# Optimization experiments

Hardware: AMD Instinct MI355X
Metric: run time of the kernel (lower is better)

The kernel has to match this reference:

```python
import jax, jax.numpy as jnp
import numpy as np

M = 28            # mask head resolution (mask_logit[i] is MxM)
NUM_CLASSES = 80  # max value of cls_idx (mask_image channel count)


def setup_inputs() -> dict:
    key = jax.random.key(0)
    k1, k2, k3, k4, k5, k6, k7 = jax.random.split(key, 7)
    N, H, W = 100, 800, 800
    cx = jax.random.uniform(k1, (N,), minval=0.0, maxval=float(W - 1))
    cy = jax.random.uniform(k2, (N,), minval=0.0, maxval=float(H - 1))
    bw = jax.random.uniform(k3, (N,), minval=20.0, maxval=300.0)
    bh = jax.random.uniform(k4, (N,), minval=20.0, maxval=300.0)
    mask_rois = jnp.stack([cx - bw / 2, cy - bh / 2, cx + bw / 2, cy + bh / 2], axis=1).astype(jnp.float32)
    cls_prob = jax.random.uniform(k5, (N,), dtype=jnp.float32)
    mask_prob = jax.random.normal(k6, (N, M, M), dtype=jnp.float32)
    cls_idx = jax.random.randint(k7, (N,), 1, NUM_CLASSES + 1, dtype=jnp.int32)
    return {"mask_rois": mask_rois, "cls_prob": cls_prob, "mask_prob": mask_prob,
            "cls_idx": cls_idx, "im_h": H, "im_w": W}


def _paste(logit, box, H, W):
    """Bilinear-paste an MxM logit into the full HxW image (== cv2.resize to (w,h)
    then placing at the box, evaluated directly on image pixel coords)."""
    x0, y0, x1, y1 = box[0], box[1], box[2], box[3]  # int32
    w = jnp.maximum(x1 - x0 + 1, 1).astype(jnp.float32)
    h = jnp.maximum(y1 - y0 + 1, 1).astype(jnp.float32)
    xs = jnp.arange(W, dtype=jnp.float32)
    ys = jnp.arange(H, dtype=jnp.float32)
    # cv2 bilinear mapping: src = (dst + 0.5) * (M / size) - 0.5, clamped at borders
    sx = jnp.clip((xs - x0.astype(jnp.float32) + 0.5) * (M / w) - 0.5, 0.0, M - 1.0)
    sy = jnp.clip((ys - y0.astype(jnp.float32) + 0.5) * (M / h) - 0.5, 0.0, M - 1.0)
    ix0 = jnp.floor(sx).astype(jnp.int32); ix1 = jnp.minimum(ix0 + 1, M - 1); fx = sx - ix0
    iy0 = jnp.floor(sy).astype(jnp.int32); iy1 = jnp.minimum(iy0 + 1, M - 1); fy = sy - iy0
    v00 = logit[iy0[:, None], ix0[None, :]]
    v01 = logit[iy0[:, None], ix1[None, :]]
    v10 = logit[iy1[:, None], ix0[None, :]]
    v11 = logit[iy1[:, None], ix1[None, :]]
    val = ((1 - fy)[:, None] * ((1 - fx)[None, :] * v00 + fx[None, :] * v01)
           + fy[:, None] * ((1 - fx)[None, :] * v10 + fx[None, :] * v11))
    xi = jnp.arange(W, dtype=jnp.int32)
    yi = jnp.arange(H, dtype=jnp.int32)
    inside_x = (xi >= jnp.maximum(x0, 0)) & (xi < jnp.minimum(x1 + 1, W))
    inside_y = (yi >= jnp.maximum(y0, 0)) & (yi < jnp.minimum(y1 + 1, H))
    inside = inside_y[:, None] & inside_x[None, :]
    return jnp.where(inside, val, 0.0), inside


def _forward(mask_rois, cls_prob, mask_prob, cls_idx, H, W, thr):
    N = mask_prob.shape[0]
    order = jnp.argsort(-cls_prob)                       # sort by score, descending
    boxes = mask_rois[order].astype(jnp.int32)
    logits = mask_prob[order]
    cls = cls_idx[order].astype(jnp.int32) - 1           # 0-based class ids
    pasted, inside = jax.vmap(lambda l, b: _paste(l, b, H, W))(logits, boxes)  # [N,H,W]

    def step(mask_image, xs):
        logit, ins, c = xs
        mask = (logit > 0) & ins                          # thresholded, in-image crop mask
        prev = mask_image[c]
        msum = jnp.sum(mask).astype(jnp.float32)
        ovl = jnp.sum(mask & prev).astype(jnp.float32)    # overlap with accumulated class mask
        keep = (msum > 0) & (ovl <= thr * msum)           # skip if ratio > threshold
        mask_image = mask_image.at[c].set(prev | (mask & keep))
        return mask_image, keep

    mask_image0 = jnp.zeros((NUM_CLASSES, H, W), dtype=bool)
    _, keep = jax.lax.scan(step, mask_image0, (pasted, inside, cls))

    # compact kept masks to the front (frame_id order); dropped boxes go to slot N (discarded)
    pos = jnp.where(keep, jnp.cumsum(keep.astype(jnp.int32)) - 1, N)
    energy = jnp.where(inside & keep[:, None, None], pasted, 0.0)
    full = jnp.zeros((N + 1, H, W), pasted.dtype).at[pos].set(energy)
    mask_energy = full[:N][None]                          # [1, N, H, W], kept masks first
    keep_inds = jnp.full((N + 1,), -1, jnp.int32).at[pos].set(
        jnp.where(keep, order.astype(jnp.int32), -1))[:N]
    return keep_inds, mask_energy


def reference(mask_rois, cls_prob, mask_prob, cls_idx, im_h, im_w):
    return _forward(mask_rois, cls_prob, mask_prob, cls_idx, int(im_h), int(im_w), 0.3)
```

## Files before the change

kernel.cpp:

```cpp
#include <hip/hip_runtime.h>

#define NINST 100
#define MLOG 28
#define IMG 800
#define LOGSZ (MLOG * MLOG)

#define OFF_ORDER 0
#define OFF_CLS   100
#define OFF_BOX   200
#define OFF_MSUM  600
#define OFF_SLOT  800
#define OFF_NK    900
#define OFF_MASK  1024
#define ROWW      12
#define MSTRIDE   (ROWW * 304)
#define PAIR_CAP  512
#define ZTOT      (IMG * IMG * NINST / 4)
#define ZBLKS     4096

__global__ __launch_bounds__(256) void k_raster(const float* __restrict__ mask_prob,
                                                const float* __restrict__ cls_prob,
                                                const float* __restrict__ rois,
                                                const int* __restrict__ cls_idx,
                                                int* __restrict__ ws) {
    int b = blockIdx.x, tid = threadIdx.x;
    __shared__ float s_p[NINST];
    __shared__ int s_order[NINST];
    __shared__ float lg[LOGSZ];
    __shared__ int red[256];
    if (tid < NINST) s_p[tid] = cls_prob[tid];
    __syncthreads();
    if (tid < NINST) {
        float p = s_p[tid];
        int r = 0;
        for (int j = 0; j < NINST; j++) {
            float q = s_p[j];
            r += (q > p) || (q == p && j < tid);
        }
        s_order[r] = tid;
    }
    __syncthreads();
    int n = b;
    int orig = s_order[n];
    int x0 = (int)rois[4 * orig], y0 = (int)rois[4 * orig + 1];
    int x1 = (int)rois[4 * orig + 2], y1 = (int)rois[4 * orig + 3];
    if (b == 0) {
        if (tid < NINST) {
            int o = s_order[tid];
            ws[OFF_ORDER + tid] = o;
            ws[OFF_CLS + tid] = cls_idx[o] - 1;
#pragma unroll
            for (int k = 0; k < 4; k++)
                ws[OFF_BOX + 4 * tid + k] = (int)rois[4 * o + k];
        }
    }
    for (int i = tid; i < LOGSZ; i += 256) lg[i] = mask_prob[orig * LOGSZ + i];
    __syncthreads();
    int xs = max(x0, 0), xe = min(x1 + 1, IMG);
    int ys = max(y0, 0), ye = min(y1 + 1, IMG);
    int wx0 = xs >> 5, nw = ((xe + 31) >> 5) - wx0, nrows = ye - ys;
    float wf = fmaxf((float)(x1 - x0 + 1), 1.f), hf = fmaxf((float)(y1 - y0 + 1), 1.f);
    float rx = 28.f / wf, ry = 28.f / hf;
    unsigned* mb = (unsigned*)(ws + OFF_MASK) + n * MSTRIDE;
    int total = nrows * nw, cnt = 0;
    for (int t = tid; t < total; t += 256) {
        int row = t / nw, wc = t - row * nw;
        int y = ys + row;
        float sy = ((float)y - (float)y0 + 0.5f) * ry - 0.5f;
        sy = fminf(fmaxf(sy, 0.f), 27.f);
        int iy0 = (int)sy, iy1 = min(iy0 + 1, 27);
        float fy = sy - (float)iy0;
        const float* r0 = lg + iy0 * MLOG;
        const float* r1 = lg + iy1 * MLOG;
        unsigned bits = 0u;
        int xbase = (wx0 + wc) << 5;
        int j0 = max(xs - xbase, 0), j1 = min(xe - xbase, 32);
        for (int j = j0; j < j1; j++) {
            int xx = xbase + j;
            float sx = ((float)xx - (float)x0 + 0.5f) * rx - 0.5f;
            sx = fminf(fmaxf(sx, 0.f), 27.f);
            int ix0 = (int)sx, ix1 = min(ix0 + 1, 27);
            float fx = sx - (float)ix0;
            float val = (1.f - fy) * ((1.f - fx) * r0[ix0] + fx * r0[ix1]) +
                        fy * ((1.f - fx) * r1[ix0] + fx * r1[ix1]);
            bits |= (val > 0.f) ? (1u << j) : 0u;
        }
        mb[row * ROWW + wc] = bits;
        cnt += __popc(bits);
    }
    red[tid] = cnt;
    __syncthreads();
    for (int s = 128; s; s >>= 1) {
        if (tid < s) red[tid] += red[tid + s];
        __syncthreads();
    }
    if (tid == 0) ws[OFF_MSUM + n] = red[0];
}

__global__ __launch_bounds__(256) void k_scan_zero(int* __restrict__ ws, float* __restrict__ out) {
    int b = blockIdx.x, tid = threadIdx.x;
    if (b > 0) {
        float4* z = (float4*)(out + NINST);
        for (size_t pi = (size_t)(b - 1) * 256 + tid; pi < (size_t)ZTOT; pi += (size_t)ZBLKS * 256)
            z[pi] = make_float4(0.f, 0.f, 0.f, 0.f);
        return;
    }
    const unsigned* maskbase = (const unsigned*)(ws + OFF_MASK);
    __shared__ int s_cls[NINST], s_msum[NINST], s_box[4 * NINST];
    __shared__ int s_wi[PAIR_CAP], s_wj[PAIR_CAP], s_po[PAIR_CAP];
    __shared__ int s_nw;
    __shared__ int s_cand[32];
    for (int i = tid; i < NINST; i += 256) {
        s_cls[i] = ws[OFF_CLS + i];
        s_msum[i] = ws[OFF_MSUM + i];
    }
    for (int i = tid; i < 4 * NINST; i += 256) s_box[i] = ws[OFF_BOX + i];
    if (tid == 0) s_nw = 0;
    __syncthreads();
    for (int c = tid; c < NINST * NINST; c += 256) {
        int i = c / NINST, j = c - i * NINST;
        if (i >= j) continue;
        if (s_cls[i] != s_cls[j]) continue;
        if (s_msum[i] == 0 || s_msum[j] == 0) continue;
        int ixs = max(s_box[4 * i], 0), ixe = min(s_box[4 * i + 2] + 1, IMG);
        int iys = max(s_box[4 * i + 1], 0), iye = min(s_box[4 * i + 3] + 1, IMG);
        int jxs = max(s_box[4 * j], 0), jxe = min(s_box[4 * j + 2] + 1, IMG);
        int jys = max(s_box[4 * j + 1], 0), jye = min(s_box[4 * j + 3] + 1, IMG);
        if (!(ixs < jxe && jxs < ixe && iys < jye && jys < iye)) continue;
        int k = atomicAdd(&s_nw, 1);
        if (k < PAIR_CAP) { s_wi[k] = i; s_wj[k] = j; }
    }
    __syncthreads();
    int nw = min(s_nw, PAIR_CAP);
    int wid = tid >> 6, lane = tid & 63;
    for (int k = wid; k < nw; k += 4) {
        int i = s_wi[k], j = s_wj[k];
        int ixs = max(s_box[4 * i], 0), ixe = min(s_box[4 * i + 2] + 1, IMG);
        int iys = max(s_box[4 * i + 1], 0), iye = min(s_box[4 * i + 3] + 1, IMG);
        int jxs = max(s_box[4 * j], 0), jxe = min(s_box[4 * j + 2] + 1, IMG);
        int jys = max(s_box[4 * j + 1], 0);
        int iwx0 = ixs >> 5, jwx0 = jxs >> 5;
        int wlo = max(iwx0, jwx0);
        int whi = min((ixe + 31) >> 5, (jxe + 31) >> 5);
        int rlo = max(iys, jys);
        int rhi = min(iye, min(s_box[4 * j + 3] + 1, IMG));
        int nwrd = whi - wlo, nrows = rhi - rlo;
        const unsigned* mi = maskbase + i * MSTRIDE;
        const unsigned* mj = maskbase + j * MSTRIDE;
        int total = nrows * nwrd, cnt = 0;
        for (int t = lane; t < total; t += 64) {
            int row = t / nwrd, wc = t - row * nwrd;
            int y = rlo + row, w = wlo + wc;
            unsigned a = mi[(y - iys) * ROWW + (w - iwx0)];
            unsigned bb = mj[(y - jys) * ROWW + (w - jwx0)];
            cnt += __popc(a & bb);
        }
        for (int off = 32; off; off >>= 1) cnt += __shfl_down(cnt, off);
        if (lane == 0) s_po[k] = cnt;
    }
    __syncthreads();
    if (tid >= 64) return;
    unsigned long long k0 = 0, k1 = 0;
    for (int n = 0; n < NINST; n++) {
        int msum = s_msum[n];
        int lsum = 0, lmax = 0, lcnt = 0;
        for (int q = lane; q < nw; q += 64) {
            if (s_wj[q] == n) {
                int pi = s_wi[q];
                bool kb = (pi < 64) ? ((k0 >> pi) & 1ull) : ((k1 >> (pi - 64)) & 1ull);
                if (kb) { int o = s_po[q]; lsum += o; lmax = max(lmax, o); lcnt++; }
            }
        }
        for (int off = 32; off; off >>= 1) {
            lsum += __shfl_xor(lsum, off);
            lmax = max(lmax, __shfl_xor(lmax, off));
            lcnt += __shfl_xor(lcnt, off);
        }
        float thr = 0.3f * (float)msum;
        int keep;
        if (lcnt == 0 || (float)lsum <= thr) keep = (msum > 0);
        else if ((float)lmax > thr) keep = 0;
        else {
            int nc = 0;
            for (int q0 = 0; q0 < nw; q0 += 64) {
                int q = q0 + lane;
                bool p = false; int piv = 0;
                if (q < nw && s_wj[q] == n) {
                    piv = s_wi[q];
                    p = (piv < 64) ? ((k0 >> piv) & 1ull) : ((k1 >> (piv - 64)) & 1ull);
                }
                unsigned long long m = __ballot(p);
                int pos = nc + __popcll(m & ((1ull << lane) - 1ull));
                if (p && pos < 32) s_cand[pos] = piv;
                nc += __popcll(m);
            }
            nc = min(nc, 32);
            asm volatile("s_waitcnt lgkmcnt(0)" ::: "memory");
            __builtin_amdgcn_sched_barrier(0);
            int nxs = max(s_box[4 * n], 0), nxe = min(s_box[4 * n + 2] + 1, IMG);
            int nys = max(s_box[4 * n + 1], 0), nye = min(s_box[4 * n + 3] + 1, IMG);
            int wx0 = nxs >> 5, nwrd = ((nxe + 31) >> 5) - wx0, nrows = nye - nys;
            const unsigned* mn = maskbase + n * MSTRIDE;
            int total = nrows * nwrd, ovl = 0;
            for (int t2 = lane; t2 < total; t2 += 64) {
                int row = t2 / nwrd, wc = t2 - row * nwrd;
                unsigned bits = mn[row * ROWW + wc];
                if (!bits) continue;
                int y = nys + row, wa = wx0 + wc;
                unsigned img = 0;
                for (int k = 0; k < nc; k++) {
                    int m2 = s_cand[k];
                    int mys = max(s_box[4 * m2 + 1], 0), mye = min(s_box[4 * m2 + 3] + 1, IMG);
                    int mxs = max(s_box[4 * m2], 0), mxe = min(s_box[4 * m2 + 2] + 1, IMG);
                    int mwx0 = mxs >> 5, mnw = ((mxe + 31) >> 5) - mwx0;
                    int rr = y - mys, cc = wa - mwx0;
                    if (rr >= 0 && rr < (mye - mys) && cc >= 0 && cc < mnw)
                        img |= maskbase[m2 * MSTRIDE + rr * ROWW + cc];
                }
                ovl += __popc(bits & img);
            }
            for (int off = 32; off; off >>= 1) ovl += __shfl_xor(ovl, off);
            keep = (msum > 0) && ((float)ovl <= thr);
        }
        if (keep) { if (n < 64) k0 |= 1ull << n; else k1 |= 1ull << (n - 64); }
    }
    if (lane == 0) {
        int nk = 0;
        for (int n = 0; n < NINST; n++) {
            bool kb = (n < 64) ? ((k0 >> n) & 1ull) : ((k1 >> (n - 64)) & 1ull);
            if (kb) {
                ws[OFF_SLOT + nk] = n;
                out[nk] = (float)ws[OFF_ORDER + n];
                nk++;
            }
        }
        ws[OFF_NK] = nk;
        for (int s2 = nk; s2 < NINST; s2++) out[s2] = -1.f;
    }
}

__global__ __launch_bounds__(256) void k_box(const float* __restrict__ mask_prob,
                                             const int* __restrict__ ws,
                                             float* __restrict__ out) {
    int slot = blockIdx.y, tid = threadIdx.x;
    if (slot >= ws[OFF_NK]) return;
    int n = ws[OFF_SLOT + slot];
    const int* box = ws + OFF_BOX + 4 * n;
    int x0 = box[0], y0 = box[1], x1 = box[2], y1 = box[3];
    int xs = max(x0, 0), xe = min(x1 + 1, IMG);
    int ys = max(y0, 0), ye = min(y1 + 1, IMG);
    int xa = xs & ~3;
    int w4 = (xe - xa + 3) >> 2;
    int rows = ye - ys;
    int total = rows * w4;
    __shared__ float lg[LOGSZ];
    int orig = ws[OFF_ORDER + n];
    for (int i = tid; i < LOGSZ; i += 256) lg[i] = mask_prob[orig * LOGSZ + i];
    __syncthreads();
    float wf = fmaxf((float)(x1 - x0 + 1), 1.f), hf = fmaxf((float)(y1 - y0 + 1), 1.f);
    float rx = 28.f / wf, ry = 28.f / hf;
    float* base = out + NINST + (size_t)slot * (IMG * IMG);
    for (int t = blockIdx.x * 256 + tid; t < total; t += gridDim.x * 256) {
        int row = t / w4, c4 = t - row * w4;
        int y = ys + row, xb = xa + (c4 << 2);
        float sy = ((float)y - (float)y0 + 0.5f) * ry - 0.5f;
        sy = fminf(fmaxf(sy, 0.f), 27.f);
        int iy0 = (int)sy, iy1 = min(iy0 + 1, 27);
        float fy = sy - (float)iy0;
        const float* r0 = lg + iy0 * MLOG;
        const float* r1 = lg + iy1 * MLOG;
        float v[4];
#pragma unroll
        for (int j = 0; j < 4; j++) {
            int xx = xb + j;
            float val = 0.f;
            if (xx >= xs && xx < xe) {
                float sx = ((float)xx - (float)x0 + 0.5f) * rx - 0.5f;
                sx = fminf(fmaxf(sx, 0.f), 27.f);
                int ix0 = (int)sx, ix1 = min(ix0 + 1, 27);
                float fx = sx - (float)ix0;
                val = (1.f - fy) * ((1.f - fx) * r0[ix0] + fx * r0[ix1]) +
                      fy * ((1.f - fx) * r1[ix0] + fx * r1[ix1]);
            }
            v[j] = val;
        }
        *(float4*)(base + (size_t)y * IMG + xb) = make_float4(v[0], v[1], v[2], v[3]);
    }
}

extern "C" void kernel_launch(void* const* d_in, const int* in_sizes, int n_in,
                              void* d_out, int out_size, void* d_ws, size_t ws_size,
                              hipStream_t stream) {
    const float* rois      = (const float*)d_in[0];
    const float* cls_prob  = (const float*)d_in[1];
    const float* mask_prob = (const float*)d_in[2];
    const int*   cls_idx   = (const int*)d_in[3];
    int* ws = (int*)d_ws;
    float* out = (float*)d_out;

    k_raster<<<dim3(NINST), dim3(256), 0, stream>>>(mask_prob, cls_prob, rois, cls_idx, ws);
    k_scan_zero<<<dim3(1 + ZBLKS), dim3(256), 0, stream>>>(ws, out);
    k_box<<<dim3(91, NINST), dim3(256), 0, stream>>>(mask_prob, ws, out);
}
```

Before: 352.2 us.

## Move pairwise overlap counting into a separate grid-parallel kernel

Pair discovery and popcount of overlapping bitmasks for same-class overlapping instances move from block 0 of the scan kernel into a new 100x100-block kernel, one wave per pair. Results are written to workspace through an atomic counter. The serial scan then keeps the pair list in per-lane registers instead of shared memory. This removes a serial bottleneck in block 0, which would otherwise delay the rest of the scan. The cost is an extra launch of 10,000 mostly-empty blocks, and pair order now depends on atomics, which appears harmless to the scan logic.

```diff
diff --git a/kernel.cpp b/kernel.cpp
--- a/kernel.cpp
+++ b/kernel.cpp
@@ -11,9 +11,11 @@
 #define OFF_MSUM  600
 #define OFF_SLOT  800
 #define OFF_NK    900
+#define OFF_NPAIR 901
 #define OFF_MASK  1024
 #define ROWW      12
 #define MSTRIDE   (ROWW * 304)
+#define OFF_PAIRS (OFF_MASK + NINST * MSTRIDE)
 #define PAIR_CAP  512
 #define ZTOT      (IMG * IMG * NINST / 4)
 #define ZBLKS     4096
@@ -45,6 +47,7 @@
     int x0 = (int)rois[4 * orig], y0 = (int)rois[4 * orig + 1];
     int x1 = (int)rois[4 * orig + 2], y1 = (int)rois[4 * orig + 3];
     if (b == 0) {
+        if (tid == 0) ws[OFF_NPAIR] = 0;
         if (tid < NINST) {
             int o = s_order[tid];
             ws[OFF_ORDER + tid] = o;
@@ -97,6 +100,44 @@
     if (tid == 0) ws[OFF_MSUM + n] = red[0];
 }
 
+__global__ __launch_bounds__(64) void k_pairs(int* __restrict__ ws) {
+    int i = blockIdx.x, j = blockIdx.y, tid = threadIdx.x;
+    if (i >= j) return;
+    if (ws[OFF_CLS + i] != ws[OFF_CLS + j]) return;
+    if (ws[OFF_MSUM + i] == 0 || ws[OFF_MSUM + j] == 0) return;
+    const int* bi = ws + OFF_BOX + 4 * i;
+    const int* bj = ws + OFF_BOX + 4 * j;
+    int ixs = max(bi[0], 0), ixe = min(bi[2] + 1, IMG);
+    int iys = max(bi[1], 0), iye = min(bi[3] + 1, IMG);
+    int jxs = max(bj[0], 0), jxe = min(bj[2] + 1, IMG);
+    int jys = max(bj[1], 0), jye = min(bj[3] + 1, IMG);
+    if (!(ixs < jxe && jxs < ixe && iys < jye && jys < iye)) return;
+    int iwx0 = ixs >> 5, jwx0 = jxs >> 5;
+    int wlo = max(iwx0, jwx0);
+    int whi = min((ixe + 31) >> 5, (jxe + 31) >> 5);
+    int rlo = max(iys, jys), rhi = min(iye, jye);
+    int nw = whi - wlo, nrows = rhi - rlo;
+    const unsigned* mi = (const unsigned*)(ws + OFF_MASK) + i * MSTRIDE;
+    const unsigned* mj = (const unsigned*)(ws + OFF_MASK) + j * MSTRIDE;
+    int total = nrows * nw, cnt = 0;
+    for (int t = tid; t < total; t += 64) {
+        int row = t / nw, wc = t - row * nw;
+        int y = rlo + row, w = wlo + wc;
+        unsigned a = mi[(y - iys) * ROWW + (w - iwx0)];
+        unsigned b = mj[(y - jys) * ROWW + (w - jwx0)];
+        cnt += __popc(a & b);
+    }
+    for (int off = 32; off; off >>= 1) cnt += __shfl_down(cnt, off);
+    if (tid == 0) {
+        int k = atomicAdd(ws + OFF_NPAIR, 1);
+        if (k < PAIR_CAP) {
+            ws[OFF_PAIRS + 3 * k] = i;
+            ws[OFF_PAIRS + 3 * k + 1] = j;
+            ws[OFF_PAIRS + 3 * k + 2] = cnt;
+        }
+    }
+}
+
 __global__ __launch_bounds__(256) void k_scan_zero(int* __restrict__ ws, float* __restrict__ out) {
     int b = blockIdx.x, tid = threadIdx.x;
     if (b > 0) {
@@ -105,70 +146,38 @@
             z[pi] = make_float4(0.f, 0.f, 0.f, 0.f);
         return;
     }
+    if (tid >= 64) return;
+    int lane = tid;
     const unsigned* maskbase = (const unsigned*)(ws + OFF_MASK);
-    __shared__ int s_cls[NINST], s_msum[NINST], s_box[4 * NINST];
-    __shared__ int s_wi[PAIR_CAP], s_wj[PAIR_CAP], s_po[PAIR_CAP];
-    __shared__ int s_nw;
+    __shared__ int s_msum[NINST];
+    __shared__ int s_box[4 * NINST];
     __shared__ int s_cand[32];
-    for (int i = tid; i < NINST; i += 256) {
-        s_cls[i] = ws[OFF_CLS + i];
-        s_msum[i] = ws[OFF_MSUM + i];
-    }
-    for (int i = tid; i < 4 * NINST; i += 256) s_box[i] = ws[OFF_BOX + i];
-    if (tid == 0) s_nw = 0;
-    __syncthreads();
-    for (int c = tid; c < NINST * NINST; c += 256) {
-        int i = c / NINST, j = c - i * NINST;
-        if (i >= j) continue;
-        if (s_cls[i] != s_cls[j]) continue;
-        if (s_msum[i] == 0 || s_msum[j] == 0) continue;
-        int ixs = max(s_box[4 * i], 0), ixe = min(s_box[4 * i + 2] + 1, IMG);
-        int iys = max(s_box[4 * i + 1], 0), iye = min(s_box[4 * i + 3] + 1, IMG);
-        int jxs = max(s_box[4 * j], 0), jxe = min(s_box[4 * j + 2] + 1, IMG);
-        int jys = max(s_box[4 * j + 1], 0), jye = min(s_box[4 * j + 3] + 1, IMG);
-        if (!(ixs < jxe && jxs < ixe && iys < jye && jys < iye)) continue;
-        int k = atomicAdd(&s_nw, 1);
-        if (k < PAIR_CAP) { s_wi[k] = i; s_wj[k] = j; }
-    }
-    __syncthreads();
-    int nw = min(s_nw, PAIR_CAP);
-    int wid = tid >> 6, lane = tid & 63;
-    for (int k = wid; k < nw; k += 4) {
-        int i = s_wi[k], j = s_wj[k];
-        int ixs = max(s_box[4 * i], 0), ixe = min(s_box[4 * i + 2] + 1, IMG);
-        int iys = max(s_box[4 * i + 1], 0), iye = min(s_box[4 * i + 3] + 1, IMG);
-        int jxs = max(s_box[4 * j], 0), jxe = min(s_box[4 * j + 2] + 1, IMG);
-        int jys = max(s_box[4 * j + 1], 0);
-        int iwx0 = ixs >> 5, jwx0 = jxs >> 5;
-        int wlo = max(iwx0, jwx0);
-        int whi = min((ixe + 31) >> 5, (jxe + 31) >> 5);
-        int rlo = max(iys, jys);
-        int rhi = min(iye, min(s_box[4 * j + 3] + 1, IMG));
-        int nwrd = whi - wlo, nrows = rhi - rlo;
-        const unsigned* mi = maskbase + i * MSTRIDE;
-        const unsigned* mj = maskbase + j * MSTRIDE;
-        int total = nrows * nwrd, cnt = 0;
-        for (int t = lane; t < total; t += 64) {
-            int row = t / nwrd, wc = t - row * nwrd;
-            int y = rlo + row, w = wlo + wc;
-            unsigned a = mi[(y - iys) * ROWW + (w - iwx0)];
-            unsigned bb = mj[(y - jys) * ROWW + (w - jwx0)];
-            cnt += __popc(a & bb);
-        }
-        for (int off = 32; off; off >>= 1) cnt += __shfl_down(cnt, off);
-        if (lane == 0) s_po[k] = cnt;
-    }
-    __syncthreads();
-    if (tid >= 64) return;
+    for (int i = lane; i < NINST; i += 64) s_msum[i] = ws[OFF_MSUM + i];
+    for (int i = lane; i < 4 * NINST; i += 64) s_box[i] = ws[OFF_BOX + i];
+    int npair = min(ws[OFF_NPAIR], PAIR_CAP);
+    int rpi[8], rpj[8], rpo[8];
+#pragma unroll
+    for (int s = 0; s < 8; s++) {
+        int q = lane + (s << 6);
+        rpi[s] = 0; rpo[s] = 0; rpj[s] = -1;
+        if (q < npair) {
+            rpi[s] = ws[OFF_PAIRS + 3 * q];
+            rpj[s] = ws[OFF_PAIRS + 3 * q + 1];
+            rpo[s] = ws[OFF_PAIRS + 3 * q + 2];
+        }
+    }
+    asm volatile("s_waitcnt vmcnt(0) lgkmcnt(0)" ::: "memory");
+    __builtin_amdgcn_sched_barrier(0);
     unsigned long long k0 = 0, k1 = 0;
     for (int n = 0; n < NINST; n++) {
         int msum = s_msum[n];
         int lsum = 0, lmax = 0, lcnt = 0;
-        for (int q = lane; q < nw; q += 64) {
-            if (s_wj[q] == n) {
-                int pi = s_wi[q];
+#pragma unroll
+        for (int s = 0; s < 8; s++) {
+            if (rpj[s] == n) {
+                int pi = rpi[s];
                 bool kb = (pi < 64) ? ((k0 >> pi) & 1ull) : ((k1 >> (pi - 64)) & 1ull);
-                if (kb) { int o = s_po[q]; lsum += o; lmax = max(lmax, o); lcnt++; }
+                if (kb) { lsum += rpo[s]; lmax = max(lmax, rpo[s]); lcnt++; }
             }
         }
         for (int off = 32; off; off >>= 1) {
@@ -182,11 +191,11 @@
         else if ((float)lmax > thr) keep = 0;
         else {
             int nc = 0;
-            for (int q0 = 0; q0 < nw; q0 += 64) {
-                int q = q0 + lane;
+#pragma unroll
+            for (int s = 0; s < 8; s++) {
                 bool p = false; int piv = 0;
-                if (q < nw && s_wj[q] == n) {
-                    piv = s_wi[q];
+                if (rpj[s] == n) {
+                    piv = rpi[s];
                     p = (piv < 64) ? ((k0 >> piv) & 1ull) : ((k1 >> (piv - 64)) & 1ull);
                 }
                 unsigned long long m = __ballot(p);
@@ -299,6 +308,7 @@
     float* out = (float*)d_out;
 
     k_raster<<<dim3(NINST), dim3(256), 0, stream>>>(mask_prob, cls_prob, rois, cls_idx, ws);
+    k_pairs<<<dim3(NINST, NINST), dim3(64), 0, stream>>>(ws);
     k_scan_zero<<<dim3(1 + ZBLKS), dim3(256), 0, stream>>>(ws, out);
     k_box<<<dim3(91, NINST), dim3(256), 0, stream>>>(mask_prob, ws, out);
 }
```

After: 346.3 us. Within noise of the previous version (-1.7%).
